# Kernel optimization log

Hardware: AMD Instinct MI355X
Metric: run time of the kernel (lower is better)

## Reference

```python
import jax, jax.numpy as jnp
import numpy as np

N_NODES = 50000
N_EDGES = 800000
IN_FEATS = 128
OUT_FEATS = 128


def mean_agg(feat, src, dst, num_nodes):
    # DGL copy_u + mean reduce: mean of in-neighbor (src) features per dst node;
    # nodes with zero in-degree get 0.
    msg = feat[src]                                        # [E, D] gather
    summed = jax.ops.segment_sum(msg, dst, num_segments=num_nodes)  # [N, D]
    deg = jax.ops.segment_sum(jnp.ones((src.shape[0],), feat.dtype), dst,
                              num_segments=num_nodes)      # [N]
    return summed / jnp.maximum(deg, 1.0)[:, None]


def setup_inputs() -> dict:
    key = jax.random.key(0)
    ks = jax.random.split(key, 16)
    sx = 1.0 / np.sqrt(IN_FEATS)
    sh = 1.0 / np.sqrt(OUT_FEATS)
    inp = {
        "x": jax.random.normal(ks[0], (N_NODES, IN_FEATS), jnp.float32),
        "h": jax.random.normal(ks[1], (N_NODES, OUT_FEATS), jnp.float32),
        "c": jax.random.normal(ks[2], (N_NODES, OUT_FEATS), jnp.float32),
        # stacked weights for the 4 gates (order: i, f, c, o)
        "Wx_self": jax.random.normal(ks[3], (4, IN_FEATS, OUT_FEATS), jnp.float32) * sx,
        "Wx_neigh": jax.random.normal(ks[4], (4, IN_FEATS, OUT_FEATS), jnp.float32) * sx,
        "Wh_self": jax.random.normal(ks[5], (4, OUT_FEATS, OUT_FEATS), jnp.float32) * sh,
        "Wh_neigh": jax.random.normal(ks[6], (4, OUT_FEATS, OUT_FEATS), jnp.float32) * sh,
        "w_ci": jax.random.uniform(ks[7], (OUT_FEATS,), jnp.float32),
        "w_cf": jax.random.uniform(ks[8], (OUT_FEATS,), jnp.float32),
        "w_co": jax.random.uniform(ks[9], (OUT_FEATS,), jnp.float32),
        "b_i": jax.random.uniform(ks[10], (OUT_FEATS,), jnp.float32),
        "b_f": jax.random.uniform(ks[11], (OUT_FEATS,), jnp.float32),
        "b_c": jax.random.uniform(ks[12], (OUT_FEATS,), jnp.float32),
        "b_o": jax.random.uniform(ks[13], (OUT_FEATS,), jnp.float32),
        "src": jax.random.randint(ks[14], (N_EDGES,), 0, N_NODES, jnp.int32),
        "dst": jax.random.randint(ks[15], (N_EDGES,), 0, N_NODES, jnp.int32),
    }
    return inp


def reference(x, h, c, Wx_self, Wx_neigh, Wh_self, Wh_neigh,
              w_ci, w_cf, w_co, b_i, b_f, b_c, b_o, src, dst):
    n = x.shape[0]
    # reuse_gate_rz=True: compute the two mean-aggregations once, shared by all nets
    h_N = mean_agg(x, src, dst, n)      # neighbor mean of x  [N, in]
    h_agg = mean_agg(h, src, dst, n)    # neighbor mean of h  [N, out]

    # each sub-net: net(g, feat, h_N=agg) = feat @ W_self + agg @ W_neigh
    # batched over the 4 gates (i, f, c, o)
    gx = jnp.einsum('ni,gio->gno', x, Wx_self) + jnp.einsum('ni,gio->gno', h_N, Wx_neigh)
    gh = jnp.einsum('no,goe->gne', h, Wh_self) + jnp.einsum('no,goe->gne', h_agg, Wh_neigh)
    s = gx + gh                          # [4, N, out]

    i = jax.nn.sigmoid(s[0] + w_ci * c + b_i)
    f = jax.nn.sigmoid(s[1] + w_cf * c + b_f)
    c_tilde = jnp.tanh(s[2] + b_c)
    new_c = f * c + i * c_tilde
    o = jax.nn.sigmoid(s[3] + w_co * new_c + b_o)
    new_h = o * jnp.tanh(new_c)
    return new_h, new_c
```

## Files before the change

### kernel.cpp

```cpp
#include <hip/hip_runtime.h>
#include <hip/hip_bf16.h>
#include <stdint.h>

#define N_NODES 50000
#define N_EDGES 800000
#define D 128
#define NPAD 50048
#define HKD 256
#define KDIM 512

typedef __attribute__((ext_vector_type(8))) __bf16 bf16x8;
typedef __attribute__((ext_vector_type(4))) __bf16 bf16x4;
typedef __attribute__((ext_vector_type(4))) float f32x4;

__device__ __forceinline__ void gload_lds16(const void* g, void* l) {
  __builtin_amdgcn_global_load_lds(
      (const __attribute__((address_space(1))) unsigned int*)(uintptr_t)g,
      (__attribute__((address_space(3))) unsigned int*)(uint32_t)(uintptr_t)l,
      16, 0, 0);
}

__device__ __forceinline__ float sigm(float v) { return 1.0f / (1.0f + __expf(-v)); }
__device__ __forceinline__ float tanh_fast(float v) { return 1.0f - 2.0f / (1.0f + __expf(2.0f * v)); }

__device__ __forceinline__ int swz(int r) { return (r & 3) ^ ((r >> 2) & 3); }

#define NB_DEG 3125
#define NB_TOB 6250
#define NB_PKW 1024
__global__ void k_pre(const int* __restrict__ dst, int* __restrict__ deg,
                      const float* __restrict__ x, const float* __restrict__ h,
                      __bf16* __restrict__ XH,
                      const float* __restrict__ Wx_self, const float* __restrict__ Wx_neigh,
                      const float* __restrict__ Wh_self, const float* __restrict__ Wh_neigh,
                      __bf16* __restrict__ W) {
  int b = blockIdx.x;
  if (b < NB_DEG) {
    int e = b * 256 + threadIdx.x;
    atomicAdd(&deg[dst[e]], 1);
  } else if (b < NB_DEG + NB_TOB) {
    int idx = (b - NB_DEG) * 256 + threadIdx.x;
    int node = idx >> 5;
    int f4 = (idx & 31) << 2;
    float4 xv = *(const float4*)(x + (size_t)node * D + f4);
    float4 hv = *(const float4*)(h + (size_t)node * D + f4);
    bf16x4 a, bb;
    a[0] = (__bf16)xv.x; a[1] = (__bf16)xv.y; a[2] = (__bf16)xv.z; a[3] = (__bf16)xv.w;
    bb[0] = (__bf16)hv.x; bb[1] = (__bf16)hv.y; bb[2] = (__bf16)hv.z; bb[3] = (__bf16)hv.w;
    __bf16* xhrow = XH + (size_t)node * HKD;
    *(bf16x4*)(xhrow + f4) = a;
    *(bf16x4*)(xhrow + 128 + f4) = bb;
  } else {
    int idx = (b - NB_DEG - NB_TOB) * 256 + threadIdx.x;
    int nq = idx >> 9, k = idx & 511;
    int g = nq >> 7, o = nq & 127;
    const float* s; int i;
    if (k < 128)      { s = Wx_self;  i = k; }
    else if (k < 256) { s = Wh_self;  i = k - 128; }
    else if (k < 384) { s = Wx_neigh; i = k - 256; }
    else              { s = Wh_neigh; i = k - 384; }
    W[idx] = (__bf16)s[(g << 14) + (i << 7) + o];
  }
}

__global__ __launch_bounds__(1024) void k_scan(const int* __restrict__ deg, int* __restrict__ offs,
                                               int* __restrict__ cursor, int n) {
  const int t = threadIdx.x;
  const int lane = t & 63;
  const int w = t >> 6;
  __shared__ int wsum[16];
  __shared__ int carry_s;
  int carry = 0;
  for (int base = 0; base < n; base += 4096) {
    int idx = base + t * 4;
    int4 v = make_int4(0, 0, 0, 0);
    if (idx < n) v = *(const int4*)(deg + idx);
    int tsum = v.x + v.y + v.z + v.w;
    int s = tsum;
#pragma unroll
    for (int d = 1; d < 64; d <<= 1) {
      int u = __shfl_up(s, d, 64);
      if (lane >= d) s += u;
    }
    if (lane == 63) wsum[w] = s;
    __syncthreads();
    int woff = 0;
    for (int i = 0; i < w; i++) woff += wsum[i];
    int excl = carry + woff + (s - tsum);
    if (idx < n) {
      int4 o;
      o.x = excl; o.y = excl + v.x; o.z = o.y + v.y; o.w = o.z + v.z;
      *(int4*)(offs + idx) = o;
      *(int4*)(cursor + idx) = o;
    }
    __syncthreads();
    if (t == 0) {
      int tot = carry;
#pragma unroll
      for (int i = 0; i < 16; i++) tot += wsum[i];
      carry_s = tot;
    }
    __syncthreads();
    carry = carry_s;
  }
  if (t == 0) offs[n] = carry;
}

__global__ void k_fill(const int* __restrict__ src, const int* __restrict__ dst,
                       int* __restrict__ cursor, int* __restrict__ bins) {
  int e = blockIdx.x * 256 + threadIdx.x;
  if (e < N_EDGES) {
    int d = dst[e];
    int p = atomicAdd(&cursor[d], 1);
    bins[p] = src[e];
  }
}

__global__ void k_gather(const int* __restrict__ offs, const int* __restrict__ bins,
                         const __bf16* __restrict__ XH, __bf16* __restrict__ ZM) {
  int wid = (blockIdx.x * 256 + threadIdx.x) >> 6;
  int lane = threadIdx.x & 63;
  if (wid >= NPAD) return;
  if (wid >= N_NODES) {
    ((uint2*)(XH + (size_t)wid * HKD))[lane] = make_uint2(0, 0);
    ((uint2*)(ZM + (size_t)wid * HKD))[lane] = make_uint2(0, 0);
    return;
  }
  const int half = lane >> 5;
  const int li = lane & 31;
  const int srcoff = li * 8;
  int beg = offs[wid], end = offs[wid + 1];
  float a[8] = {0.f, 0.f, 0.f, 0.f, 0.f, 0.f, 0.f, 0.f};
  for (int j = beg + half; j < end; j += 2) {
    int s = bins[j];
    bf16x8 v = *(const bf16x8*)(XH + (size_t)s * HKD + srcoff);
#pragma unroll
    for (int e = 0; e < 8; ++e) a[e] += (float)v[e];
  }
#pragma unroll
  for (int e = 0; e < 8; ++e) a[e] += __shfl_xor(a[e], 32, 64);
  int degn = end - beg;
  float inv = 1.0f / (float)(degn > 0 ? degn : 1);
  if (lane < 32) {
    bf16x8 bb;
#pragma unroll
    for (int e = 0; e < 8; ++e) bb[e] = (__bf16)(a[e] * inv);
    *(bf16x8*)(ZM + (size_t)wid * HKD + srcoff) = bb;
  }
}

__global__ __launch_bounds__(256, 4) void k_gemm(
    const __bf16* __restrict__ XH, const __bf16* __restrict__ ZM, const __bf16* __restrict__ W,
    const float* __restrict__ c,
    const float* __restrict__ w_ci, const float* __restrict__ w_cf, const float* __restrict__ w_co,
    const float* __restrict__ b_i, const float* __restrict__ b_f, const float* __restrict__ b_c,
    const float* __restrict__ b_o,
    float* __restrict__ out_h, float* __restrict__ out_c) {
  __shared__ __align__(16) __bf16 As[64 * 32];
  __shared__ __align__(16) __bf16 Bs[256 * 32];
  const int t = threadIdx.x;
  const int lane = t & 63;
  const int w = t >> 6;
  const int m0 = (blockIdx.x >> 1) * 64;
  const int o0 = (blockIdx.x & 1) * 64;
  const int l15 = lane & 15;
  const int q = lane >> 4;

  f32x4 acc[4][4];
#pragma unroll
  for (int m = 0; m < 4; ++m)
#pragma unroll
    for (int g = 0; g < 4; ++g) acc[m][g] = (f32x4){0.f, 0.f, 0.f, 0.f};

  const int arow = t >> 2, aslot = t & 3;
  const size_t aoff = (size_t)(m0 + arow) * HKD + ((aslot ^ swz(arow)) << 3);
  const __bf16* bSrc[4];
#pragma unroll
  for (int j = 0; j < 4; ++j) {
    int l = j * 256 + t;
    int brow = l >> 2, bslot = l & 3;
    int wrow = (brow >> 6) * 128 + o0 + (brow & 63);
    bSrc[j] = W + (size_t)wrow * KDIM + ((bslot ^ swz(brow)) << 3);
  }

  for (int k0 = 0; k0 < KDIM; k0 += 32) {
    const __bf16* sA = (k0 < 256) ? (XH + aoff + k0) : (ZM + aoff + (k0 - 256));
    gload_lds16(sA, (__bf16*)As + t * 8);
#pragma unroll
    for (int j = 0; j < 4; ++j)
      gload_lds16(bSrc[j] + k0, (__bf16*)Bs + (j * 256 + t) * 8);
    __syncthreads();

    bf16x8 af[4], bfr[4];
#pragma unroll
    for (int m = 0; m < 4; ++m) {
      int row = m * 16 + l15;
      af[m] = *(const bf16x8*)(As + row * 32 + ((q ^ swz(row)) << 3));
    }
#pragma unroll
    for (int g = 0; g < 4; ++g) {
      int n = g * 64 + w * 16 + l15;
      bfr[g] = *(const bf16x8*)(Bs + n * 32 + ((q ^ swz(n)) << 3));
    }
#pragma unroll
    for (int m = 0; m < 4; ++m)
#pragma unroll
      for (int g = 0; g < 4; ++g)
        acc[m][g] = __builtin_amdgcn_mfma_f32_16x16x32_bf16(af[m], bfr[g], acc[m][g], 0, 0, 0);
    __syncthreads();
  }

  const int o = o0 + w * 16 + l15;
  const float wci = w_ci[o], wcf = w_cf[o], wco = w_co[o];
  const float bi = b_i[o], bfv = b_f[o], bc = b_c[o], bo = b_o[o];
#pragma unroll
  for (int m = 0; m < 4; ++m) {
#pragma unroll
    for (int r = 0; r < 4; ++r) {
      int row = m0 + m * 16 + q * 4 + r;
      if (row < N_NODES) {
        float cv = c[(size_t)row * D + o];
        float ig = sigm(acc[m][0][r] + wci * cv + bi);
        float fg = sigm(acc[m][1][r] + wcf * cv + bfv);
        float ct = tanh_fast(acc[m][2][r] + bc);
        float nc = fg * cv + ig * ct;
        float og = sigm(acc[m][3][r] + wco * nc + bo);
        out_h[(size_t)row * D + o] = og * tanh_fast(nc);
        out_c[(size_t)row * D + o] = nc;
      }
    }
  }
}

extern "C" void kernel_launch(void* const* d_in, const int* in_sizes, int n_in,
                              void* d_out, int out_size, void* d_ws, size_t ws_size,
                              hipStream_t stream) {
  const float* x = (const float*)d_in[0];
  const float* h = (const float*)d_in[1];
  const float* c = (const float*)d_in[2];
  const float* Wx_self = (const float*)d_in[3];
  const float* Wx_neigh = (const float*)d_in[4];
  const float* Wh_self = (const float*)d_in[5];
  const float* Wh_neigh = (const float*)d_in[6];
  const float* w_ci = (const float*)d_in[7];
  const float* w_cf = (const float*)d_in[8];
  const float* w_co = (const float*)d_in[9];
  const float* b_i = (const float*)d_in[10];
  const float* b_f = (const float*)d_in[11];
  const float* b_c = (const float*)d_in[12];
  const float* b_o = (const float*)d_in[13];
  const int* src = (const int*)d_in[14];
  const int* dst = (const int*)d_in[15];

  char* ws = (char*)d_ws;
  int* deg = (int*)(ws);
  int* offs = (int*)(ws + 200704);
  int* cursor = (int*)(ws + 400896);
  int* bins = (int*)(ws + 601088);
  __bf16* XH = (__bf16*)(ws + 4194304);
  __bf16* ZM = (__bf16*)(ws + 29818880);
  __bf16* W = (__bf16*)(ws + 55443456);

  float* out_h = (float*)d_out;
  float* out_c = out_h + (size_t)N_NODES * D;

  hipMemsetAsync(deg, 0, N_NODES * sizeof(int), stream);
  k_pre<<<NB_DEG + NB_TOB + NB_PKW, 256, 0, stream>>>(dst, deg, x, h, XH,
                                                      Wx_self, Wx_neigh, Wh_self, Wh_neigh, W);
  k_scan<<<1, 1024, 0, stream>>>(deg, offs, cursor, N_NODES);
  k_fill<<<(N_EDGES + 255) / 256, 256, 0, stream>>>(src, dst, cursor, bins);
  k_gather<<<NPAD / 4, 256, 0, stream>>>(offs, bins, XH, ZM);
  k_gemm<<<(NPAD / 64) * 2, 256, 0, stream>>>(XH, ZM, W, c, w_ci, w_cf, w_co,
                                              b_i, b_f, b_c, b_o, out_h, out_c);
}
```

Measured before the change: 242.2 us.

## Double-buffer LDS tiles in fused LSTM gate GEMM to overlap loads with MFMA

Splits the GEMM's shared-memory A and B tiles into two buffers. The next k-slice is issued with async global-to-LDS loads while MFMAs run on the current slice, and partial vmcnt waits let the in-flight loads continue. This targets the load-then-compute stall of the single-buffered loop. It doubles LDS use per block (to about 40KB), which may reduce occupancy at 4 blocks per CU, and it depends on hand-counted vmcnt values.

```diff
diff --git a/kernel.cpp b/kernel.cpp
--- a/kernel.cpp
+++ b/kernel.cpp
@@ -156,8 +156,8 @@
     const float* __restrict__ b_i, const float* __restrict__ b_f, const float* __restrict__ b_c,
     const float* __restrict__ b_o,
     float* __restrict__ out_h, float* __restrict__ out_c) {
-  __shared__ __align__(16) __bf16 As[64 * 32];
-  __shared__ __align__(16) __bf16 Bs[256 * 32];
+  __shared__ __align__(16) __bf16 As[2][64 * 32];
+  __shared__ __align__(16) __bf16 Bs[2][256 * 32];
   const int t = threadIdx.x;
   const int lane = t & 63;
   const int w = t >> 6;
@@ -183,32 +183,64 @@
     bSrc[j] = W + (size_t)wrow * KDIM + ((bslot ^ swz(brow)) << 3);
   }
 
-  for (int k0 = 0; k0 < KDIM; k0 += 32) {
+  auto STAGE = [&](int buf, int k0) {
     const __bf16* sA = (k0 < 256) ? (XH + aoff + k0) : (ZM + aoff + (k0 - 256));
-    gload_lds16(sA, (__bf16*)As + t * 8);
+    gload_lds16(sA, &As[buf][t * 8]);
 #pragma unroll
     for (int j = 0; j < 4; ++j)
-      gload_lds16(bSrc[j] + k0, (__bf16*)Bs + (j * 256 + t) * 8);
-    __syncthreads();
-
+      gload_lds16(bSrc[j] + k0, &Bs[buf][(j * 256 + t) * 8]);
+  };
+
+  auto COMPUTE = [&](int buf) {
     bf16x8 af[4], bfr[4];
 #pragma unroll
     for (int m = 0; m < 4; ++m) {
       int row = m * 16 + l15;
-      af[m] = *(const bf16x8*)(As + row * 32 + ((q ^ swz(row)) << 3));
+      af[m] = *(const bf16x8*)(&As[buf][row * 32 + ((q ^ swz(row)) << 3)]);
     }
 #pragma unroll
     for (int g = 0; g < 4; ++g) {
       int n = g * 64 + w * 16 + l15;
-      bfr[g] = *(const bf16x8*)(Bs + n * 32 + ((q ^ swz(n)) << 3));
+      bfr[g] = *(const bf16x8*)(&Bs[buf][n * 32 + ((q ^ swz(n)) << 3)]);
     }
 #pragma unroll
     for (int m = 0; m < 4; ++m)
 #pragma unroll
       for (int g = 0; g < 4; ++g)
         acc[m][g] = __builtin_amdgcn_mfma_f32_16x16x32_bf16(af[m], bfr[g], acc[m][g], 0, 0, 0);
-    __syncthreads();
-  }
+  };
+
+  STAGE(0, 0);
+  __builtin_amdgcn_sched_barrier(0);
+  for (int kk2 = 0; kk2 < 7; ++kk2) {
+    STAGE(1, 64 * kk2 + 32);
+    asm volatile("s_waitcnt vmcnt(5)" ::: "memory");
+    __builtin_amdgcn_s_barrier();
+    __builtin_amdgcn_sched_barrier(0);
+    COMPUTE(0);
+    __builtin_amdgcn_sched_barrier(0);
+    __builtin_amdgcn_s_barrier();
+
+    STAGE(0, 64 * kk2 + 64);
+    asm volatile("s_waitcnt vmcnt(5)" ::: "memory");
+    __builtin_amdgcn_s_barrier();
+    __builtin_amdgcn_sched_barrier(0);
+    COMPUTE(1);
+    __builtin_amdgcn_sched_barrier(0);
+    __builtin_amdgcn_s_barrier();
+  }
+  STAGE(1, 480);
+  asm volatile("s_waitcnt vmcnt(5)" ::: "memory");
+  __builtin_amdgcn_s_barrier();
+  __builtin_amdgcn_sched_barrier(0);
+  COMPUTE(0);
+  __builtin_amdgcn_sched_barrier(0);
+  __builtin_amdgcn_s_barrier();
+  asm volatile("s_waitcnt vmcnt(0)" ::: "memory");
+  __builtin_amdgcn_s_barrier();
+  __builtin_amdgcn_sched_barrier(0);
+  COMPUTE(1);
+  __builtin_amdgcn_sched_barrier(0);
 
   const int o = o0 + w * 16 + l15;
   const float wci = w_ci[o], wcf = w_cf[o], wco = w_co[o];
```

Result: no change. 241.3 us (-0.4%).

## Restructure GEMM: full-K A tile in LDS, prepacked W fragments from registers

Applied to the files above, without the earlier changes.

The weight matrix is now prepacked in MFMA fragment order so each wave loads its B fragments straight from global memory into registers, with double buffering. The whole 64x512 A tile is staged into swizzled LDS once, and each block covers all 128 outputs with 8 waves. This removes the per-k-step barriers and the repeated B staging through LDS, and halves how often A is reloaded. The gather loop is also unrolled by two with separate accumulators so more loads are in flight. In exchange each block uses 64 KB of LDS and more registers, which may lower occupancy, and every block re-reads W from cache.

```diff
diff --git a/kernel.cpp b/kernel.cpp
--- a/kernel.cpp
+++ b/kernel.cpp
@@ -22,8 +22,6 @@
 
 __device__ __forceinline__ float sigm(float v) { return 1.0f / (1.0f + __expf(-v)); }
 __device__ __forceinline__ float tanh_fast(float v) { return 1.0f - 2.0f / (1.0f + __expf(2.0f * v)); }
-
-__device__ __forceinline__ int swz(int r) { return (r & 3) ^ ((r >> 2) & 3); }
 
 #define NB_DEG 3125
 #define NB_TOB 6250
@@ -33,7 +31,7 @@
                       __bf16* __restrict__ XH,
                       const float* __restrict__ Wx_self, const float* __restrict__ Wx_neigh,
                       const float* __restrict__ Wh_self, const float* __restrict__ Wh_neigh,
-                      __bf16* __restrict__ W) {
+                      __bf16* __restrict__ Wp) {
   int b = blockIdx.x;
   if (b < NB_DEG) {
     int e = b * 256 + threadIdx.x;
@@ -52,14 +50,20 @@
     *(bf16x4*)(xhrow + 128 + f4) = bb;
   } else {
     int idx = (b - NB_DEG - NB_TOB) * 256 + threadIdx.x;
-    int nq = idx >> 9, k = idx & 511;
-    int g = nq >> 7, o = nq & 127;
-    const float* s; int i;
-    if (k < 128)      { s = Wx_self;  i = k; }
-    else if (k < 256) { s = Wh_self;  i = k - 128; }
-    else if (k < 384) { s = Wx_neigh; i = k - 256; }
-    else              { s = Wh_neigh; i = k - 384; }
-    W[idx] = (__bf16)s[(g << 14) + (i << 7) + o];
+    int e = idx & 7;
+    int r16 = (idx >> 3) & 15;
+    int q = (idx >> 7) & 3;
+    int s = (idx >> 9) & 15;
+    int G = idx >> 13;
+    int wrow = G * 16 + r16;
+    int g = wrow >> 7, o = wrow & 127;
+    int k = s * 32 + q * 8 + e;
+    const float* src; int i;
+    if (k < 128)      { src = Wx_self;  i = k; }
+    else if (k < 256) { src = Wh_self;  i = k - 128; }
+    else if (k < 384) { src = Wx_neigh; i = k - 256; }
+    else              { src = Wh_neigh; i = k - 384; }
+    Wp[idx] = (__bf16)src[(g << 14) + (i << 7) + o];
   }
 }
 
@@ -131,14 +135,27 @@
   const int srcoff = li * 8;
   int beg = offs[wid], end = offs[wid + 1];
   float a[8] = {0.f, 0.f, 0.f, 0.f, 0.f, 0.f, 0.f, 0.f};
-  for (int j = beg + half; j < end; j += 2) {
-    int s = bins[j];
-    bf16x8 v = *(const bf16x8*)(XH + (size_t)s * HKD + srcoff);
-#pragma unroll
-    for (int e = 0; e < 8; ++e) a[e] += (float)v[e];
-  }
-#pragma unroll
-  for (int e = 0; e < 8; ++e) a[e] += __shfl_xor(a[e], 32, 64);
+  float a2[8] = {0.f, 0.f, 0.f, 0.f, 0.f, 0.f, 0.f, 0.f};
+  int j = beg + half;
+  for (; j + 2 < end; j += 4) {
+    int s0 = bins[j];
+    int s1 = bins[j + 2];
+    bf16x8 v0 = *(const bf16x8*)(XH + (size_t)s0 * HKD + srcoff);
+    bf16x8 v1 = *(const bf16x8*)(XH + (size_t)s1 * HKD + srcoff);
+#pragma unroll
+    for (int e = 0; e < 8; ++e) { a[e] += (float)v0[e]; a2[e] += (float)v1[e]; }
+  }
+  if (j < end) {
+    int s0 = bins[j];
+    bf16x8 v0 = *(const bf16x8*)(XH + (size_t)s0 * HKD + srcoff);
+#pragma unroll
+    for (int e = 0; e < 8; ++e) a[e] += (float)v0[e];
+  }
+#pragma unroll
+  for (int e = 0; e < 8; ++e) {
+    a[e] += a2[e];
+    a[e] += __shfl_xor(a[e], 32, 64);
+  }
   int degn = end - beg;
   float inv = 1.0f / (float)(degn > 0 ? degn : 1);
   if (lane < 32) {
@@ -149,68 +166,87 @@
   }
 }
 
-__global__ __launch_bounds__(256, 4) void k_gemm(
-    const __bf16* __restrict__ XH, const __bf16* __restrict__ ZM, const __bf16* __restrict__ W,
+__global__ __launch_bounds__(512, 4) void k_gemm(
+    const __bf16* __restrict__ XH, const __bf16* __restrict__ ZM, const __bf16* __restrict__ Wp,
     const float* __restrict__ c,
     const float* __restrict__ w_ci, const float* __restrict__ w_cf, const float* __restrict__ w_co,
     const float* __restrict__ b_i, const float* __restrict__ b_f, const float* __restrict__ b_c,
     const float* __restrict__ b_o,
     float* __restrict__ out_h, float* __restrict__ out_c) {
-  __shared__ __align__(16) __bf16 As[64 * 32];
-  __shared__ __align__(16) __bf16 Bs[256 * 32];
+  __shared__ __align__(16) __bf16 As[64 * KDIM];
   const int t = threadIdx.x;
   const int lane = t & 63;
   const int w = t >> 6;
-  const int m0 = (blockIdx.x >> 1) * 64;
-  const int o0 = (blockIdx.x & 1) * 64;
+  const int m0 = blockIdx.x * 64;
   const int l15 = lane & 15;
   const int q = lane >> 4;
 
+#pragma unroll
+  for (int i = 0; i < 8; ++i) {
+    int s = i * 512 + t;
+    int row = s >> 6;
+    int cg = (s & 63) ^ (row & 7);
+    const __bf16* src = (cg < 32) ? (XH + (size_t)(m0 + row) * HKD + cg * 8)
+                                  : (ZM + (size_t)(m0 + row) * HKD + (cg - 32) * 8);
+    gload_lds16(src, (__bf16*)As + s * 8);
+  }
+  __syncthreads();
+
   f32x4 acc[4][4];
 #pragma unroll
   for (int m = 0; m < 4; ++m)
 #pragma unroll
     for (int g = 0; g < 4; ++g) acc[m][g] = (f32x4){0.f, 0.f, 0.f, 0.f};
 
-  const int arow = t >> 2, aslot = t & 3;
-  const size_t aoff = (size_t)(m0 + arow) * HKD + ((aslot ^ swz(arow)) << 3);
-  const __bf16* bSrc[4];
-#pragma unroll
-  for (int j = 0; j < 4; ++j) {
-    int l = j * 256 + t;
-    int brow = l >> 2, bslot = l & 3;
-    int wrow = (brow >> 6) * 128 + o0 + (brow & 63);
-    bSrc[j] = W + (size_t)wrow * KDIM + ((bslot ^ swz(brow)) << 3);
-  }
-
-  for (int k0 = 0; k0 < KDIM; k0 += 32) {
-    const __bf16* sA = (k0 < 256) ? (XH + aoff + k0) : (ZM + aoff + (k0 - 256));
-    gload_lds16(sA, (__bf16*)As + t * 8);
-#pragma unroll
-    for (int j = 0; j < 4; ++j)
-      gload_lds16(bSrc[j] + k0, (__bf16*)Bs + (j * 256 + t) * 8);
-    __syncthreads();
-
-    bf16x8 af[4], bfr[4];
-#pragma unroll
-    for (int m = 0; m < 4; ++m) {
-      int row = m * 16 + l15;
-      af[m] = *(const bf16x8*)(As + row * 32 + ((q ^ swz(row)) << 3));
-    }
-#pragma unroll
-    for (int g = 0; g < 4; ++g) {
-      int n = g * 64 + w * 16 + l15;
-      bfr[g] = *(const bf16x8*)(Bs + n * 32 + ((q ^ swz(n)) << 3));
-    }
-#pragma unroll
-    for (int m = 0; m < 4; ++m)
+  const __bf16* wp = Wp + (size_t)(w * 16) * 512 + lane * 8;
+
+  bf16x8 bA[4], bB[4];
+#pragma unroll
+  for (int g = 0; g < 4; ++g) bA[g] = *(const bf16x8*)(wp + g * 65536);
+
+#pragma unroll
+  for (int s2 = 0; s2 < 8; ++s2) {
+    {
+      const int step = 2 * s2;
 #pragma unroll
       for (int g = 0; g < 4; ++g)
-        acc[m][g] = __builtin_amdgcn_mfma_f32_16x16x32_bf16(af[m], bfr[g], acc[m][g], 0, 0, 0);
-    __syncthreads();
-  }
-
-  const int o = o0 + w * 16 + l15;
+        bB[g] = *(const bf16x8*)(wp + g * 65536 + (step + 1) * 512);
+      bf16x8 af[4];
+#pragma unroll
+      for (int m = 0; m < 4; ++m) {
+        int row = m * 16 + l15;
+        int cl = (step * 4 + q) ^ (row & 7);
+        af[m] = *(const bf16x8*)(As + (row * 64 + cl) * 8);
+      }
+#pragma unroll
+      for (int m = 0; m < 4; ++m)
+#pragma unroll
+        for (int g = 0; g < 4; ++g)
+          acc[m][g] = __builtin_amdgcn_mfma_f32_16x16x32_bf16(af[m], bA[g], acc[m][g], 0, 0, 0);
+    }
+    {
+      const int step = 2 * s2 + 1;
+      if (step < 15) {
+#pragma unroll
+        for (int g = 0; g < 4; ++g)
+          bA[g] = *(const bf16x8*)(wp + g * 65536 + (step + 1) * 512);
+      }
+      bf16x8 af[4];
+#pragma unroll
+      for (int m = 0; m < 4; ++m) {
+        int row = m * 16 + l15;
+        int cl = (step * 4 + q) ^ (row & 7);
+        af[m] = *(const bf16x8*)(As + (row * 64 + cl) * 8);
+      }
+#pragma unroll
+      for (int m = 0; m < 4; ++m)
+#pragma unroll
+        for (int g = 0; g < 4; ++g)
+          acc[m][g] = __builtin_amdgcn_mfma_f32_16x16x32_bf16(af[m], bB[g], acc[m][g], 0, 0, 0);
+    }
+  }
+
+  const int o = w * 16 + l15;
   const float wci = w_ci[o], wcf = w_cf[o], wco = w_co[o];
   const float bi = b_i[o], bfv = b_f[o], bc = b_c[o], bo = b_o[o];
 #pragma unroll
@@ -259,17 +295,17 @@
   int* bins = (int*)(ws + 601088);
   __bf16* XH = (__bf16*)(ws + 4194304);
   __bf16* ZM = (__bf16*)(ws + 29818880);
-  __bf16* W = (__bf16*)(ws + 55443456);
+  __bf16* Wp = (__bf16*)(ws + 55443456);
 
   float* out_h = (float*)d_out;
   float* out_c = out_h + (size_t)N_NODES * D;
 
   hipMemsetAsync(deg, 0, N_NODES * sizeof(int), stream);
   k_pre<<<NB_DEG + NB_TOB + NB_PKW, 256, 0, stream>>>(dst, deg, x, h, XH,
-                                                      Wx_self, Wx_neigh, Wh_self, Wh_neigh, W);
+                                                      Wx_self, Wx_neigh, Wh_self, Wh_neigh, Wp);
   k_scan<<<1, 1024, 0, stream>>>(deg, offs, cursor, N_NODES);
   k_fill<<<(N_EDGES + 255) / 256, 256, 0, stream>>>(src, dst, cursor, bins);
   k_gather<<<NPAD / 4, 256, 0, stream>>>(offs, bins, XH, ZM);
-  k_gemm<<<(NPAD / 64) * 2, 256, 0, stream>>>(XH, ZM, W, c, w_ci, w_cf, w_co,
-                                              b_i, b_f, b_c, b_o, out_h, out_c);
-}
+  k_gemm<<<NPAD / 64, 512, 0, stream>>>(XH, ZM, Wp, c, w_ci, w_cf, w_co,
+                                        b_i, b_f, b_c, b_o, out_h, out_c);
+}
```

Result: faster. 229.2 us (-5.4%).
